# Kernel optimization log

Hardware: AMD Instinct MI355X
Metric: run time of the kernel (lower is better)

## Reference

```python
import jax, jax.numpy as jnp
import numpy as np
import math

H = 16          # n_heads
D = 1024        # hidden_dim
HD = D // H     # head_dim = 64
LR = 256        # Linformer low-rank length L
MAX_T = 4096    # max_seq_len


def setup_inputs() -> dict:
    key = jax.random.key(0)
    ks = jax.random.split(key, 7)
    X = jax.random.normal(ks[0], (4, 4096, D), dtype=jnp.float32)
    # lecun_normal ~ N(0, 1/fan_in)
    W_kernel = jax.random.normal(ks[1], (D, 3 * D), dtype=jnp.float32) / math.sqrt(D)
    W_bias = jnp.zeros((3 * D,), dtype=jnp.float32)
    low_rank_E = jax.random.normal(ks[2], (MAX_T, H, LR), dtype=jnp.float32) / math.sqrt(MAX_T)
    low_rank_V = jax.random.normal(ks[3], (MAX_T, H, LR), dtype=jnp.float32) / math.sqrt(MAX_T)
    o_kernel = jax.random.normal(ks[4], (D, D), dtype=jnp.float32) / math.sqrt(D)
    o_bias = jnp.zeros((D,), dtype=jnp.float32)
    return {"X": X, "W_kernel": W_kernel, "W_bias": W_bias,
            "low_rank_E": low_rank_E, "low_rank_V": low_rank_V,
            "o_kernel": o_kernel, "o_bias": o_bias}


def reference(X, W_kernel, W_bias, low_rank_E, low_rank_V, o_kernel, o_bias):
    B, T, _ = X.shape
    # L2-normalize tokens
    norm = jnp.linalg.norm(X, ord=2, axis=-1, keepdims=True)  # (B,T,1)
    Xn = X / norm
    # fused QKV projection
    qkv = Xn @ W_kernel + W_bias                 # (B,T,3D)
    qkv = qkv.reshape(B, T, 3, H, HD)
    Q, K, V = qkv[:, :, 0], qkv[:, :, 1], qkv[:, :, 2]   # (B,T,H,HD)
    # low-rank sequence projection of K/V: T -> L
    E = low_rank_E[:T]                            # (T,H,L)
    F = low_rank_V[:T]                            # (T,H,L)
    Kp = jnp.einsum('THK,BTHD->BHKD', E, K)       # (B,H,L,HD)
    Vp = jnp.einsum('THK,BTHD->BHKD', F, V)       # (B,H,L,HD)
    Qh = Q.transpose(0, 2, 1, 3)                  # (B,H,T,HD)
    logits = jnp.einsum('BHTD,BHKD->BHTK', Qh, Kp) / math.sqrt(HD)
    attn = jax.nn.softmax(logits, axis=-1)        # (B,H,T,L)
    out = jnp.einsum('BHTK,BHKD->BHTD', attn, Vp) # (B,H,T,HD)
    out = out.transpose(0, 2, 1, 3).reshape(B, T, H * HD)
    return out @ o_kernel + o_bias
```

## Files before the change

### kernel.cpp

```cpp
#include <hip/hip_runtime.h>
#include <stdint.h>

typedef unsigned short u16;
typedef uint32_t u32;
typedef __bf16 bf16x8 __attribute__((ext_vector_type(8)));
typedef float f32x4 __attribute__((ext_vector_type(4)));

__device__ __forceinline__ u16 f2bf(float f) {
    u32 u = __builtin_bit_cast(u32, f);
    u += 0x7fffu + ((u >> 16) & 1u);
    return (u16)(u >> 16);
}

__device__ __forceinline__ f32x4 mfma16(bf16x8 a, bf16x8 b, f32x4 c) {
    return __builtin_amdgcn_mfma_f32_16x16x32_bf16(a, b, c, 0, 0, 0);
}

__device__ __forceinline__ void gld_lds16(void* lds, const void* g) {
    __builtin_amdgcn_global_load_lds(
        (__attribute__((address_space(1))) void*)(uintptr_t)g,
        (__attribute__((address_space(3))) void*)(u32)(uintptr_t)lds,
        16, 0, 0);
}

__global__ __launch_bounds__(256) void k_norm(const float* __restrict__ X,
                                              u16* __restrict__ Xn) {
    const int row = blockIdx.x;
    const float4 v = ((const float4*)(X + (size_t)row * 1024))[threadIdx.x];
    float ss = v.x * v.x + v.y * v.y + v.z * v.z + v.w * v.w;
#pragma unroll
    for (int m = 1; m < 64; m <<= 1) ss += __shfl_xor(ss, m);
    __shared__ float red[4];
    if ((threadIdx.x & 63) == 0) red[threadIdx.x >> 6] = ss;
    __syncthreads();
    const float sc = 1.0f / sqrtf(red[0] + red[1] + red[2] + red[3]);
    ushort4 o;
    o.x = f2bf(v.x * sc); o.y = f2bf(v.y * sc);
    o.z = f2bf(v.z * sc); o.w = f2bf(v.w * sc);
    ((ushort4*)(Xn + (size_t)row * 1024))[threadIdx.x] = o;
}

__global__ __launch_bounds__(256) void k_transpose_cast64(
    const float* __restrict__ src, u16* __restrict__ dst,
    int R, int rstride, long zsrc, long zdst) {
    __shared__ float tile[64][65];
    src += (size_t)blockIdx.z * zsrc;
    dst += (size_t)blockIdx.z * zdst;
    const int c0 = blockIdx.x * 64, r0 = blockIdx.y * 64;
    const int tid = threadIdx.x;
    const int lr = tid >> 4, lc = tid & 15;
#pragma unroll
    for (int i = 0; i < 4; ++i) {
        const int r = lr + i * 16;
        const float4 v = *(const float4*)(src + (size_t)(r0 + r) * rstride + c0 + lc * 4);
        tile[r][lc * 4 + 0] = v.x; tile[r][lc * 4 + 1] = v.y;
        tile[r][lc * 4 + 2] = v.z; tile[r][lc * 4 + 3] = v.w;
    }
    __syncthreads();
    const int c = tid >> 2, seg = tid & 3;
    u32 w[8];
#pragma unroll
    for (int j = 0; j < 8; ++j) {
        const u32 lo = f2bf(tile[seg * 16 + 2 * j][c]);
        const u32 hi = f2bf(tile[seg * 16 + 2 * j + 1][c]);
        w[j] = lo | (hi << 16);
    }
    u16* dp = dst + (size_t)(c0 + c) * R + r0 + seg * 16;
    uint4 q0; q0.x = w[0]; q0.y = w[1]; q0.z = w[2]; q0.w = w[3];
    uint4 q1; q1.x = w[4]; q1.y = w[5]; q1.z = w[6]; q1.w = w[7];
    *(uint4*)dp = q0;
    *((uint4*)dp + 1) = q1;
}

#define G8_PRE(Aptr, Bptr)                                                       \
    const int tid = threadIdx.x, lane = tid & 63;                                \
    const int wid = tid >> 6, wm = wid >> 2, wn = wid & 3;                       \
    const int cl = lane & 15, g = lane >> 4;                                     \
    const int colb = (tid & 7) * 16;                                             \
    const int scb = colb ^ (((tid >> 3) & 7) << 4);                              \
    const int rbA = ((tid >> 3) & 31) + ((tid >> 8) << 7);                       \
    const int rbB = tid >> 3;                                                    \
    const char* gA = (const char*)(Aptr) + (size_t)(m0 + rbA) * 2048 + scb;      \
    const char* gB = (const char*)(Bptr) + (size_t)(n0 + rbB) * 2048 + scb;      \
    const u32 lA = (u32)(rbA * 128 + colb);                                      \
    const u32 lB = (u32)(65536 + rbB * 128 + colb);                              \
    const int xr0 = (g * 16) ^ ((cl & 7) << 4);                                  \
    const int xr1 = (64 + g * 16) ^ ((cl & 7) << 4);

#define G8_STA(q, tau, beta) gld_lds16(sm + (beta) + lA + (q) * 4096,            \
                                       gA + (q) * 65536 + (size_t)(tau) * 128);
#define G8_STB(c, tau, beta) gld_lds16(sm + (beta) + lB + (c) * 8192,            \
                                       gB + (c) * 131072 + (size_t)(tau) * 128);

#define G8_RDB(beta)                                                             \
    _Pragma("unroll") for (int nf = 0; nf < 4; ++nf) {                           \
        const u32 rb_ = (beta) + 65536 + (u32)(wn * 64 + nf * 16 + cl) * 128;    \
        bF[nf][0] = *(const bf16x8*)(sm + rb_ + xr0);                            \
        bF[nf][1] = *(const bf16x8*)(sm + rb_ + xr1);                            \
    }
#define G8_RDA(q, beta)                                                          \
    _Pragma("unroll") for (int m = 0; m < 2; ++m) {                              \
        const u32 ra_ = (beta) + (u32)(wm * 128 + (q) * 32 + m * 16 + cl) * 128; \
        aF[m][0] = *(const bf16x8*)(sm + ra_ + xr0);                             \
        aF[m][1] = *(const bf16x8*)(sm + ra_ + xr1);                             \
    }

#define G8_MMA(q)                                                                \
    asm volatile("s_waitcnt lgkmcnt(0)" ::: "memory");                           \
    __builtin_amdgcn_sched_barrier(0);                                           \
    __builtin_amdgcn_s_setprio(1);                                               \
    _Pragma("unroll") for (int m = 0; m < 2; ++m)                                \
        _Pragma("unroll") for (int nf = 0; nf < 4; ++nf) {                       \
            acc[(q)*2 + m][nf] = mfma16(aF[m][0], bF[nf][0], acc[(q)*2 + m][nf]);\
            acc[(q)*2 + m][nf] = mfma16(aF[m][1], bF[nf][1], acc[(q)*2 + m][nf]);\
        }                                                                        \
    __builtin_amdgcn_s_setprio(0);                                               \
    __builtin_amdgcn_s_barrier();                                                \
    __builtin_amdgcn_sched_barrier(0);

#define G8_LOOP                                                                  \
    bf16x8 aF[2][2], bF[4][2];                                                   \
    G8_STA(0, 0, 0) G8_STB(0, 0, 0) G8_STA(1, 0, 0) G8_STB(1, 0, 0)              \
    G8_STA(2, 0, 0) G8_STB(2, 0, 0) G8_STA(3, 0, 0) G8_STB(3, 0, 0)              \
    G8_STA(0, 1, 32768) G8_STB(0, 1, 32768)                                      \
    G8_STA(1, 1, 32768) G8_STB(1, 1, 32768)                                      \
    G8_STA(2, 1, 32768) G8_STB(2, 1, 32768)                                      \
    for (int it = 0; it < 8; ++it) {                                             \
        const int t1 = 2 * it + 1, t2v = 2 * it + 2, t3v = 2 * it + 3;           \
        const bool nt = (it < 7);                                                \
                                                                         \
        G8_STA(3, t1, 32768) G8_STB(3, t1, 32768)                                \
        asm volatile("s_waitcnt vmcnt(8)" ::: "memory");                         \
        __builtin_amdgcn_s_barrier();                                            \
        G8_RDB(0) G8_RDA(0, 0) G8_MMA(0)                                         \
                                                                         \
        if (nt) { G8_STA(0, t2v, 0) G8_STB(0, t2v, 0) }                          \
        G8_RDA(1, 0) G8_MMA(1)                                                   \
                                                                         \
        if (nt) { G8_STA(1, t2v, 0) G8_STB(1, t2v, 0) }                          \
        G8_RDA(2, 0) G8_MMA(2)                                                   \
                                                                         \
        if (nt) { G8_STA(2, t2v, 0) G8_STB(2, t2v, 0) }                          \
        G8_RDA(3, 0) G8_MMA(3)                                                   \
                                                                         \
        if (nt) {                                                                \
            G8_STA(3, t2v, 0) G8_STB(3, t2v, 0)                                  \
            asm volatile("s_waitcnt vmcnt(8)" ::: "memory");                     \
        } else {                                                                 \
            asm volatile("s_waitcnt vmcnt(0)" ::: "memory");                     \
        }                                                                        \
        __builtin_amdgcn_s_barrier();                                            \
        G8_RDB(32768) G8_RDA(0, 32768) G8_MMA(0)                                 \
                                                                         \
        if (nt) { G8_STA(0, t3v, 32768) G8_STB(0, t3v, 32768) }                  \
        G8_RDA(1, 32768) G8_MMA(1)                                               \
                                                                         \
        if (nt) { G8_STA(1, t3v, 32768) G8_STB(1, t3v, 32768) }                  \
        G8_RDA(2, 32768) G8_MMA(2)                                               \
                                                                         \
        if (nt) { G8_STA(2, t3v, 32768) G8_STB(2, t3v, 32768) }                  \
        G8_RDA(3, 32768) G8_MMA(3)                                               \
    }

__global__ __launch_bounds__(512, 2) void k_gemm_qkv(
    const u16* __restrict__ A, const u16* __restrict__ Bt,
    const float* __restrict__ bias,
    u16* __restrict__ Qo, u16* __restrict__ Kt, u16* __restrict__ Vt) {
    __shared__ __align__(16) char sm[131072];
    u32 bid = blockIdx.x;
    bid = (bid & 7) * 96 + (bid >> 3);
    const int m0 = (int)(bid / 12) * 256, n0 = (int)(bid % 12) * 256;

    G8_PRE(A, Bt)

    const f32x4 fz = {0.f, 0.f, 0.f, 0.f};
    f32x4 acc[8][4];
#pragma unroll
    for (int i = 0; i < 8; ++i)
#pragma unroll
        for (int j = 0; j < 4; ++j) acc[i][j] = fz;

    G8_LOOP

#pragma unroll
    for (int mf = 0; mf < 8; ++mf) {
        const int mbase = m0 + wm * 128 + mf * 16 + g * 4;
        const int b = mbase >> 12;
        const int t = mbase & 4095;
#pragma unroll
        for (int nf = 0; nf < 4; ++nf) {
            const int n = n0 + wn * 64 + nf * 16 + cl;
            const float bv = bias[n];
            const int seg = n >> 10;
            const int hd = n & 1023;
            f32x4 v = acc[mf][nf];
            if (seg == 0) {
#pragma unroll
                for (int r = 0; r < 4; ++r)
                    Qo[(size_t)(mbase + r) * 1024 + hd] = f2bf(v[r] + bv);
            } else {
                u16* dst = (seg == 1) ? Kt : Vt;
                ushort4 pk;
                pk.x = f2bf(v[0] + bv); pk.y = f2bf(v[1] + bv);
                pk.z = f2bf(v[2] + bv); pk.w = f2bf(v[3] + bv);
                *(ushort4*)(dst + (size_t)(b * 1024 + hd) * 4096 + t) = pk;
            }
        }
    }
}

__global__ __launch_bounds__(512, 2) void k_gemm_out(
    const u16* __restrict__ A, const u16* __restrict__ Bt,
    const float* __restrict__ bias, float* __restrict__ out) {
    __shared__ __align__(16) char sm[131072];
    u32 bid = blockIdx.x;
    bid = (bid & 7) * 32 + (bid >> 3);
    const int m0 = (int)(bid / 4) * 256, n0 = (int)(bid % 4) * 256;

    G8_PRE(A, Bt)

    const f32x4 fz = {0.f, 0.f, 0.f, 0.f};
    f32x4 acc[8][4];
#pragma unroll
    for (int i = 0; i < 8; ++i)
#pragma unroll
        for (int j = 0; j < 4; ++j) acc[i][j] = fz;

    G8_LOOP

#pragma unroll
    for (int mf = 0; mf < 8; ++mf) {
        const int mbase = m0 + wm * 128 + mf * 16 + g * 4;
#pragma unroll
        for (int nf = 0; nf < 4; ++nf) {
            const int n = n0 + wn * 64 + nf * 16 + cl;
            const float bv = bias[n];
            f32x4 v = acc[mf][nf];
#pragma unroll
            for (int r = 0; r < 4; ++r)
                out[(size_t)(mbase + r) * 1024 + n] = v[r] + bv;
        }
    }
}

__global__ __launch_bounds__(256) void k_gemm_kpvp(
    const u16* __restrict__ Et, const u16* __restrict__ Ft,
    const u16* __restrict__ Kt, const u16* __restrict__ Vt,
    u16* __restrict__ Kp, u16* __restrict__ Vpt) {
    __shared__ __align__(16) char sm[24576];
    const int tid = threadIdx.x, lane = tid & 63, wid = tid >> 6;
    const int wm = wid >> 1, wn = wid & 1;
    const int cl = lane & 15, g = lane >> 4;
    const int mT = blockIdx.x;
    const int bh = blockIdx.y;
    const int h = bh & 15;
    const int s = blockIdx.z;

    const u16* Abase = (s == 0 ? Et : Ft) + (size_t)h * (256 * 4096);
    const u16* Bbase = (s == 0 ? Kt : Vt) + (size_t)bh * (64 * 4096);
    const u16* gA0 = Abase + (size_t)(mT * 128 + (tid >> 2)) * 4096 + (tid & 3) * 8;
    const u16* gA1 = gA0 + (size_t)64 * 4096;
    const u16* gB0 = Bbase + (size_t)(tid >> 2) * 4096 + (tid & 3) * 8;

    const f32x4 fz = {0.f, 0.f, 0.f, 0.f};
    f32x4 acc[4][2];
#pragma unroll
    for (int i = 0; i < 4; ++i) { acc[i][0] = fz; acc[i][1] = fz; }

    gld_lds16(sm + tid * 16, gA0); gld_lds16(sm + 4096 + tid * 16, gA1);
    gld_lds16(sm + 8192 + tid * 16, gB0);
    gA0 += 32; gA1 += 32; gB0 += 32;

    u32 roff = 0;
    for (int k0 = 0; k0 < 4096; k0 += 32) {
        const u32 woff = roff ^ 12288;
        if (k0 + 32 < 4096) {
            gld_lds16(sm + woff + tid * 16, gA0); gld_lds16(sm + woff + 4096 + tid * 16, gA1);
            gld_lds16(sm + woff + 8192 + tid * 16, gB0);
            gA0 += 32; gA1 += 32; gB0 += 32;
            asm volatile("s_waitcnt vmcnt(3)" ::: "memory");
        } else {
            asm volatile("s_waitcnt vmcnt(0)" ::: "memory");
        }
        __builtin_amdgcn_s_barrier();
        __builtin_amdgcn_sched_barrier(0);
        const char* rb = sm + roff;
        bf16x8 aF[4], bF[2];
#pragma unroll
        for (int mf = 0; mf < 4; ++mf)
            aF[mf] = *(const bf16x8*)(rb + (wm * 64 + mf * 16 + cl) * 64 + g * 16);
#pragma unroll
        for (int nf = 0; nf < 2; ++nf)
            bF[nf] = *(const bf16x8*)(rb + 8192 + (wn * 32 + nf * 16 + cl) * 64 + g * 16);
#pragma unroll
        for (int mf = 0; mf < 4; ++mf)
#pragma unroll
            for (int nf = 0; nf < 2; ++nf)
                acc[mf][nf] = mfma16(aF[mf], bF[nf], acc[mf][nf]);
        asm volatile("s_waitcnt lgkmcnt(0)" ::: "memory");
        __builtin_amdgcn_s_barrier();
        roff = woff;
    }

    const size_t obase = (size_t)bh * 16384;
#pragma unroll
    for (int mf = 0; mf < 4; ++mf) {
        const int m = mT * 128 + wm * 64 + mf * 16 + g * 4;
#pragma unroll
        for (int nf = 0; nf < 2; ++nf) {
            const int n = wn * 32 + nf * 16 + cl;
            f32x4 v = acc[mf][nf];
            if (s == 0) {
#pragma unroll
                for (int r = 0; r < 4; ++r)
                    Kp[obase + (size_t)(m + r) * 64 + n] = f2bf(v[r]);
            } else {
                ushort4 pk;
                pk.x = f2bf(v[0]); pk.y = f2bf(v[1]);
                pk.z = f2bf(v[2]); pk.w = f2bf(v[3]);
                *(ushort4*)(Vpt + obase + (size_t)n * 256 + m) = pk;
            }
        }
    }
}

__global__ __launch_bounds__(256, 1) void k_attn(
    const u16* __restrict__ Q, const u16* __restrict__ Kp,
    const u16* __restrict__ Vpt, u16* __restrict__ AO) {
    __shared__ __align__(16) char sm[65536];
    const int lane = threadIdx.x & 63, wid = threadIdx.x >> 6;
    const int cl = lane & 15, g = lane >> 4;
    const int tT = blockIdx.x, h = blockIdx.y, b = blockIdx.z;
    const int bh = b * 16 + h;
    const int trow0 = b * 4096 + tT * 128 + wid * 32;
    const u16* Qb = Q + (size_t)trow0 * 1024 + h * 64;
    const u16* KpB = Kp + (size_t)bh * (256 * 64);
    const u16* VpB = Vpt + (size_t)bh * (64 * 256);
    char* sP = sm + wid * 16384;

    bf16x8 qF[2][2];
#pragma unroll
    for (int nf = 0; nf < 2; ++nf)
#pragma unroll
        for (int ks = 0; ks < 2; ++ks)
            qF[nf][ks] = *(const bf16x8*)(Qb + (size_t)(nf * 16 + cl) * 1024 + ks * 32 + g * 8);

    const f32x4 fz = {0.f, 0.f, 0.f, 0.f};
    f32x4 Sp[16][2];
#pragma unroll
    for (int mf = 0; mf < 16; ++mf) { Sp[mf][0] = fz; Sp[mf][1] = fz; }

#pragma unroll
    for (int mf = 0; mf < 16; ++mf) {
#pragma unroll
        for (int ks = 0; ks < 2; ++ks) {
            bf16x8 aF = *(const bf16x8*)(KpB + (size_t)(mf * 16 + cl) * 64 + ks * 32 + g * 8);
            Sp[mf][0] = mfma16(aF, qF[0][ks], Sp[mf][0]);
            Sp[mf][1] = mfma16(aF, qF[1][ks], Sp[mf][1]);
        }
    }

    float inv_sum[2];
#pragma unroll
    for (int nf = 0; nf < 2; ++nf) {
        float mx = -1e30f;
#pragma unroll
        for (int mf = 0; mf < 16; ++mf)
#pragma unroll
            for (int r = 0; r < 4; ++r) {
                float x = Sp[mf][nf][r] * 0.125f;
                Sp[mf][nf][r] = x;
                mx = fmaxf(mx, x);
            }
        mx = fmaxf(mx, __shfl_xor(mx, 16));
        mx = fmaxf(mx, __shfl_xor(mx, 32));
        float sum = 0.f;
#pragma unroll
        for (int mf = 0; mf < 16; ++mf)
#pragma unroll
            for (int r = 0; r < 4; ++r) {
                float p = __expf(Sp[mf][nf][r] - mx);
                Sp[mf][nf][r] = p;
                sum += p;
            }
        sum += __shfl_xor(sum, 16);
        sum += __shfl_xor(sum, 32);
        inv_sum[nf] = 1.0f / sum;

        const int tl = nf * 16 + cl;
        const int sw = (tl & 7) << 4;
#pragma unroll
        for (int mf = 0; mf < 16; ++mf) {
            uint2 pk;
            pk.x = (u32)f2bf(Sp[mf][nf][0]) | ((u32)f2bf(Sp[mf][nf][1]) << 16);
            pk.y = (u32)f2bf(Sp[mf][nf][2]) | ((u32)f2bf(Sp[mf][nf][3]) << 16);
            *(uint2*)(sP + ((tl * 512 + (mf * 16 + g * 4) * 2) ^ sw)) = pk;
        }
    }

    f32x4 Oa[4][2];
#pragma unroll
    for (int mf = 0; mf < 4; ++mf) { Oa[mf][0] = fz; Oa[mf][1] = fz; }
#pragma unroll
    for (int ks = 0; ks < 8; ++ks) {
        bf16x8 aF[4];
#pragma unroll
        for (int mf = 0; mf < 4; ++mf)
            aF[mf] = *(const bf16x8*)(VpB + (size_t)(mf * 16 + cl) * 256 + ks * 32 + g * 8);
#pragma unroll
        for (int nf = 0; nf < 2; ++nf) {
            const int tl = nf * 16 + cl;
            const int sw = (tl & 7) << 4;
            bf16x8 bF = *(const bf16x8*)(sP + ((tl * 512 + (ks * 32 + g * 8) * 2) ^ sw));
#pragma unroll
            for (int mf = 0; mf < 4; ++mf)
                Oa[mf][nf] = mfma16(aF[mf], bF, Oa[mf][nf]);
        }
    }

#pragma unroll
    for (int nf = 0; nf < 2; ++nf) {
        const int t = trow0 + nf * 16 + cl;
#pragma unroll
        for (int mf = 0; mf < 4; ++mf) {
            f32x4 v = Oa[mf][nf];
            ushort4 pk;
            pk.x = f2bf(v[0] * inv_sum[nf]); pk.y = f2bf(v[1] * inv_sum[nf]);
            pk.z = f2bf(v[2] * inv_sum[nf]); pk.w = f2bf(v[3] * inv_sum[nf]);
            *(ushort4*)(AO + (size_t)t * 1024 + h * 64 + mf * 16 + g * 4) = pk;
        }
    }
}

extern "C" void kernel_launch(void* const* d_in, const int* in_sizes, int n_in,
                              void* d_out, int out_size, void* d_ws, size_t ws_size,
                              hipStream_t stream) {
    const float* X  = (const float*)d_in[0];
    const float* Wk = (const float*)d_in[1];
    const float* Wb = (const float*)d_in[2];
    const float* E  = (const float*)d_in[3];
    const float* F  = (const float*)d_in[4];
    const float* Ok = (const float*)d_in[5];
    const float* Ob = (const float*)d_in[6];
    float* out = (float*)d_out;
    char* ws = (char*)d_ws;

    u16* Xn  = (u16*)(ws + 0);
    u16* Wt  = (u16*)(ws + 33554432);
    u16* Ot  = (u16*)(ws + 39845888);
    u16* Et  = (u16*)(ws + 41943040);
    u16* Ft  = (u16*)(ws + 75497472);
    u16* Qb  = (u16*)(ws + 109051904);
    u16* Kt  = (u16*)(ws + 142606336);
    u16* Vt  = (u16*)(ws + 176160768);
    u16* Kp  = (u16*)(ws + 209715200);
    u16* Vpt = (u16*)(ws + 211812352);
    u16* AO  = Xn;

    k_norm<<<16384, 256, 0, stream>>>(X, Xn);
    k_transpose_cast64<<<dim3(48, 16, 1), 256, 0, stream>>>(Wk, Wt, 1024, 3072, 0, 0);
    k_transpose_cast64<<<dim3(16, 16, 1), 256, 0, stream>>>(Ok, Ot, 1024, 1024, 0, 0);
    k_transpose_cast64<<<dim3(4, 64, 16), 256, 0, stream>>>(E, Et, 4096, 4096, 256, 1048576);
    k_transpose_cast64<<<dim3(4, 64, 16), 256, 0, stream>>>(F, Ft, 4096, 4096, 256, 1048576);
    k_gemm_qkv<<<768, 512, 0, stream>>>(Xn, Wt, Wb, Qb, Kt, Vt);
    k_gemm_kpvp<<<dim3(2, 64, 2), 256, 0, stream>>>(Et, Ft, Kt, Vt, Kp, Vpt);
    k_attn<<<dim3(32, 16, 4), 256, 0, stream>>>(Qb, Kp, Vpt, AO);
    k_gemm_out<<<256, 512, 0, stream>>>(AO, Ot, Ob, out);
}
```

Before: 387.7 us.

## Split-K the low-rank K/V projection with batch-concatenated tiles and reduction

Restructures the E^T·K / F^T·V projection GEMM so each block covers all four batches for one head (N=256), sharing the E/F tile across batches. The K dimension is split four ways to raise block count, and fp32 partials are written to workspace and summed by a new reduction kernel that also casts to bf16 and produces the Kp/Vpt layouts. It adds an XOR swizzle on LDS tiles to avoid bank conflicts and raises MFMA priority. In exchange it costs an extra kernel launch and fp32 partial traffic, and the Vpt stores in the reduction are strided.

Result: faster. 375.3 us (-3.2%).

```diff
diff --git a/kernel.cpp b/kernel.cpp
--- a/kernel.cpp
+++ b/kernel.cpp
@@ -243,41 +243,52 @@
     }
 }
 
-__global__ __launch_bounds__(256) void k_gemm_kpvp(
+__global__ __launch_bounds__(512) void k_gemm_kpvp(
     const u16* __restrict__ Et, const u16* __restrict__ Ft,
     const u16* __restrict__ Kt, const u16* __restrict__ Vt,
-    u16* __restrict__ Kp, u16* __restrict__ Vpt) {
-    __shared__ __align__(16) char sm[24576];
+    float* __restrict__ Pp) {
+    __shared__ __align__(16) char sm[49152];
     const int tid = threadIdx.x, lane = tid & 63, wid = tid >> 6;
-    const int wm = wid >> 1, wn = wid & 1;
+    const int wm = wid >> 2, wn = wid & 3;
     const int cl = lane & 15, g = lane >> 4;
     const int mT = blockIdx.x;
-    const int bh = blockIdx.y;
-    const int h = bh & 15;
-    const int s = blockIdx.z;
-
-    const u16* Abase = (s == 0 ? Et : Ft) + (size_t)h * (256 * 4096);
-    const u16* Bbase = (s == 0 ? Kt : Vt) + (size_t)bh * (64 * 4096);
-    const u16* gA0 = Abase + (size_t)(mT * 128 + (tid >> 2)) * 4096 + (tid & 3) * 8;
-    const u16* gA1 = gA0 + (size_t)64 * 4096;
-    const u16* gB0 = Bbase + (size_t)(tid >> 2) * 4096 + (tid & 3) * 8;
+    const int hs = blockIdx.y;
+    const int h = hs & 15, s = hs >> 4;
+    const int ks = blockIdx.z;
+
+    const u16* Ab = (s ? Ft : Et) + (size_t)h * (256 * 4096)
+                    + (size_t)(mT * 128) * 4096 + ks * 1024;
+    const u16* Bb = s ? Vt : Kt;
+
+    const int rA = tid >> 2, c16 = tid & 3;
+    const int scol = (c16 ^ ((rA >> 1) & 3)) * 8;
+    const u16* gA = Ab + (size_t)rA * 4096 + scol;
+    const int rB1 = rA + 128;
+    const u16* gB0 = Bb + (size_t)((((rA >> 6) * 16 + h) * 64) + (rA & 63)) * 4096
+                     + ks * 1024 + scol;
+    const u16* gB1 = Bb + (size_t)((((rB1 >> 6) * 16 + h) * 64) + (rB1 & 63)) * 4096
+                     + ks * 1024 + scol;
+    const u32 lA = (u32)(rA * 64 + c16 * 16);
+    const u32 lB0 = (u32)(8192 + rA * 64 + c16 * 16);
+    const u32 lB1 = (u32)(8192 + rB1 * 64 + c16 * 16);
+    const int xsw = (g ^ ((cl >> 1) & 3)) * 16;
 
     const f32x4 fz = {0.f, 0.f, 0.f, 0.f};
-    f32x4 acc[4][2];
-#pragma unroll
-    for (int i = 0; i < 4; ++i) { acc[i][0] = fz; acc[i][1] = fz; }
-
-    gld_lds16(sm + tid * 16, gA0); gld_lds16(sm + 4096 + tid * 16, gA1);
-    gld_lds16(sm + 8192 + tid * 16, gB0);
-    gA0 += 32; gA1 += 32; gB0 += 32;
+    f32x4 acc[4][4];
+#pragma unroll
+    for (int i = 0; i < 4; ++i)
+#pragma unroll
+        for (int j = 0; j < 4; ++j) acc[i][j] = fz;
+
+    gld_lds16(sm + lA, gA); gld_lds16(sm + lB0, gB0); gld_lds16(sm + lB1, gB1);
 
     u32 roff = 0;
-    for (int k0 = 0; k0 < 4096; k0 += 32) {
-        const u32 woff = roff ^ 12288;
-        if (k0 + 32 < 4096) {
-            gld_lds16(sm + woff + tid * 16, gA0); gld_lds16(sm + woff + 4096 + tid * 16, gA1);
-            gld_lds16(sm + woff + 8192 + tid * 16, gB0);
-            gA0 += 32; gA1 += 32; gB0 += 32;
+    for (int kt = 0; kt < 32; ++kt) {
+        const u32 woff = roff ^ 24576;
+        if (kt < 31) {
+            gld_lds16(sm + woff + lA, gA + (kt + 1) * 32);
+            gld_lds16(sm + woff + lB0, gB0 + (kt + 1) * 32);
+            gld_lds16(sm + woff + lB1, gB1 + (kt + 1) * 32);
             asm volatile("s_waitcnt vmcnt(3)" ::: "memory");
         } else {
             asm volatile("s_waitcnt vmcnt(0)" ::: "memory");
@@ -285,42 +296,68 @@
         __builtin_amdgcn_s_barrier();
         __builtin_amdgcn_sched_barrier(0);
         const char* rb = sm + roff;
-        bf16x8 aF[4], bF[2];
+        bf16x8 aF[4], bF[4];
 #pragma unroll
         for (int mf = 0; mf < 4; ++mf)
-            aF[mf] = *(const bf16x8*)(rb + (wm * 64 + mf * 16 + cl) * 64 + g * 16);
-#pragma unroll
-        for (int nf = 0; nf < 2; ++nf)
-            bF[nf] = *(const bf16x8*)(rb + 8192 + (wn * 32 + nf * 16 + cl) * 64 + g * 16);
+            aF[mf] = *(const bf16x8*)(rb + (wm * 64 + mf * 16 + cl) * 64 + xsw);
+#pragma unroll
+        for (int nf = 0; nf < 4; ++nf)
+            bF[nf] = *(const bf16x8*)(rb + 8192 + (wn * 64 + nf * 16 + cl) * 64 + xsw);
+        asm volatile("s_waitcnt lgkmcnt(0)" ::: "memory");
+        __builtin_amdgcn_sched_barrier(0);
+        __builtin_amdgcn_s_setprio(1);
 #pragma unroll
         for (int mf = 0; mf < 4; ++mf)
 #pragma unroll
-            for (int nf = 0; nf < 2; ++nf)
+            for (int nf = 0; nf < 4; ++nf)
                 acc[mf][nf] = mfma16(aF[mf], bF[nf], acc[mf][nf]);
+        __builtin_amdgcn_s_setprio(0);
         asm volatile("s_waitcnt lgkmcnt(0)" ::: "memory");
         __builtin_amdgcn_s_barrier();
         roff = woff;
     }
 
-    const size_t obase = (size_t)bh * 16384;
+    float* P = Pp + ((size_t)(ks * 32 + hs) << 16);
 #pragma unroll
     for (int mf = 0; mf < 4; ++mf) {
         const int m = mT * 128 + wm * 64 + mf * 16 + g * 4;
 #pragma unroll
-        for (int nf = 0; nf < 2; ++nf) {
-            const int n = wn * 32 + nf * 16 + cl;
+        for (int nf = 0; nf < 4; ++nf) {
+            const int dcat = wn * 64 + nf * 16 + cl;
             f32x4 v = acc[mf][nf];
-            if (s == 0) {
-#pragma unroll
-                for (int r = 0; r < 4; ++r)
-                    Kp[obase + (size_t)(m + r) * 64 + n] = f2bf(v[r]);
-            } else {
-                ushort4 pk;
-                pk.x = f2bf(v[0]); pk.y = f2bf(v[1]);
-                pk.z = f2bf(v[2]); pk.w = f2bf(v[3]);
-                *(ushort4*)(Vpt + obase + (size_t)n * 256 + m) = pk;
-            }
-        }
+#pragma unroll
+            for (int r = 0; r < 4; ++r)
+                P[(size_t)(m + r) * 256 + dcat] = v[r];
+        }
+    }
+}
+
+__global__ __launch_bounds__(256) void k_red(const float* __restrict__ Pp,
+                                             u16* __restrict__ Kp,
+                                             u16* __restrict__ Vpt) {
+    const int e = blockIdx.x * 256 + threadIdx.x;
+    const int hs = e >> 14;
+    const int rem = (e & 16383) * 4;
+    float4 sum = {0.f, 0.f, 0.f, 0.f};
+#pragma unroll
+    for (int ks = 0; ks < 4; ++ks) {
+        const float4 v = *(const float4*)(Pp + (((size_t)(ks * 32 + hs)) << 16) + rem);
+        sum.x += v.x; sum.y += v.y; sum.z += v.z; sum.w += v.w;
+    }
+    const int m = rem >> 8, dcat = rem & 255;
+    const int h = hs & 15, sf = hs >> 4;
+    const int bh = (dcat >> 6) * 16 + h, d0 = dcat & 63;
+    if (sf == 0) {
+        ushort4 pk;
+        pk.x = f2bf(sum.x); pk.y = f2bf(sum.y);
+        pk.z = f2bf(sum.z); pk.w = f2bf(sum.w);
+        *(ushort4*)(Kp + (size_t)bh * 16384 + m * 64 + d0) = pk;
+    } else {
+        u16* vp = Vpt + (size_t)bh * 16384 + m;
+        vp[(d0 + 0) * 256] = f2bf(sum.x);
+        vp[(d0 + 1) * 256] = f2bf(sum.y);
+        vp[(d0 + 2) * 256] = f2bf(sum.z);
+        vp[(d0 + 3) * 256] = f2bf(sum.w);
     }
 }
 
@@ -455,6 +492,7 @@
     u16* Vt  = (u16*)(ws + 176160768);
     u16* Kp  = (u16*)(ws + 209715200);
     u16* Vpt = (u16*)(ws + 211812352);
+    float* Pp = (float*)(ws + 0);
     u16* AO  = Xn;
 
     k_norm<<<16384, 256, 0, stream>>>(X, Xn);
@@ -463,7 +501,8 @@
     k_transpose_cast64<<<dim3(4, 64, 16), 256, 0, stream>>>(E, Et, 4096, 4096, 256, 1048576);
     k_transpose_cast64<<<dim3(4, 64, 16), 256, 0, stream>>>(F, Ft, 4096, 4096, 256, 1048576);
     k_gemm_qkv<<<768, 512, 0, stream>>>(Xn, Wt, Wb, Qb, Kt, Vt);
-    k_gemm_kpvp<<<dim3(2, 64, 2), 256, 0, stream>>>(Et, Ft, Kt, Vt, Kp, Vpt);
+    k_gemm_kpvp<<<dim3(2, 32, 4), 512, 0, stream>>>(Et, Ft, Kt, Vt, Pp);
+    k_red<<<2048, 256, 0, stream>>>(Pp, Kp, Vpt);
     k_attn<<<dim3(32, 16, 4), 256, 0, stream>>>(Qb, Kp, Vpt, AO);
     k_gemm_out<<<256, 512, 0, stream>>>(AO, Ot, Ob, out);
 }
```
